# Performance work log

Hardware: AMD Instinct MI355X
Metric: run time of the kernel (lower is better)

## Reference

```python
import jax, jax.numpy as jnp
import numpy as np

INPUT_DIM, HIDDEN, OUTPUT_DIM, NUM_LAYERS = 512, 128, 96, 5
BATCH, SEQ = 64, 512


def _gru_layer(x_seq, w_ih, w_hh, b_ih, b_hh):
    """Single GRU layer, PyTorch gate conventions. x_seq: [B,T,I] -> [B,T,H]."""
    B = x_seq.shape[0]
    H = w_hh.shape[1]
    # Precompute input-to-hidden gates for all timesteps: [B,T,3H]
    gx = jnp.einsum('bti,gi->btg', x_seq, w_ih) + b_ih

    def step(h, gx_t):
        gh = h @ w_hh.T + b_hh                      # [B,3H]
        xr, xz, xn = jnp.split(gx_t, 3, axis=-1)
        hr, hz, hn = jnp.split(gh, 3, axis=-1)
        r = jax.nn.sigmoid(xr + hr)
        z = jax.nn.sigmoid(xz + hz)
        n = jnp.tanh(xn + r * hn)
        h_new = (1.0 - z) * n + z * h
        return h_new, h_new

    h0 = jnp.zeros((B, H), x_seq.dtype)
    _, hs = jax.lax.scan(step, h0, jnp.swapaxes(gx, 0, 1))  # [T,B,H]
    return jnp.swapaxes(hs, 0, 1)                           # [B,T,H]


def setup_inputs() -> dict:
    key = jax.random.key(0)
    ks = jax.random.split(key, 8)
    s = 1.0 / np.sqrt(HIDDEN)  # torch default uniform init bound
    u = lambda k, shape: jax.random.uniform(k, shape, jnp.float32, -s, s)
    return {
        'x': jax.random.normal(ks[0], (BATCH, SEQ, INPUT_DIM), jnp.float32),
        'w_ih0': u(ks[1], (3 * HIDDEN, INPUT_DIM)),
        'w_ih_rest': u(ks[2], (NUM_LAYERS - 1, 3 * HIDDEN, HIDDEN)),
        'w_hh': u(ks[3], (NUM_LAYERS, 3 * HIDDEN, HIDDEN)),
        'b_ih': u(ks[4], (NUM_LAYERS, 3 * HIDDEN)),
        'b_hh': u(ks[5], (NUM_LAYERS, 3 * HIDDEN)),
        'fc_w': u(ks[6], (OUTPUT_DIM, HIDDEN)),
        'fc_b': u(ks[7], (OUTPUT_DIM,)),
    }


def reference(x, w_ih0, w_ih_rest, w_hh, b_ih, b_hh, fc_w, fc_b):
    h = _gru_layer(x, w_ih0, w_hh[0], b_ih[0], b_hh[0])
    for l in range(1, NUM_LAYERS):
        h = _gru_layer(h, w_ih_rest[l - 1], w_hh[l], b_ih[l], b_hh[l])
    # final linear on last timestep: [B,H] -> [B,OUTPUT_DIM]
    return h[:, -1, :] @ fc_w.T + fc_b
```

## Files before the change

### kernel.cpp

```cpp
#include <hip/hip_runtime.h>
#include <hip/hip_bf16.h>

#define BATCH   64
#define SEQ     512
#define IN0     512
#define HID     128
#define G3      384
#define NLAY    5
#define CHUNK   8

typedef _Float16 f16x8 __attribute__((ext_vector_type(8)));
typedef float    f32x4 __attribute__((ext_vector_type(4)));

static __device__ __forceinline__ float sigf(float x) {
    return __builtin_amdgcn_rcpf(1.f + __expf(-x));
}
static __device__ __forceinline__ float tanh_fast(float x) {
    const float e = __expf(-2.f * fabsf(x));
    return copysignf((1.f - e) * __builtin_amdgcn_rcpf(1.f + e), x);
}

__global__ __launch_bounds__(256) void gemm_gx(const float* __restrict__ A,
                                               const float* __restrict__ W,
                                               const float* __restrict__ bias,
                                               float* __restrict__ gx)
{
    __shared__ __align__(16) _Float16 As[64][40];
    __shared__ __align__(16) _Float16 Bs[64][40];

    const int tid  = threadIdx.x;
    const int lane = tid & 63;
    const int wv   = tid >> 6;
    const int n16  = lane & 15;
    const int quad = lane >> 4;
    const int row0 = blockIdx.x * 64;
    const int col0 = blockIdx.y * 64;
    const int r    = tid >> 2;
    const int kc   = (tid & 3) * 8;

    f32x4 acc[4];
    #pragma unroll
    for (int nt = 0; nt < 4; nt++) acc[nt] = (f32x4){0.f, 0.f, 0.f, 0.f};

    for (int k0 = 0; k0 < IN0; k0 += 32) {
        {
            const float* Ap = A + (size_t)(row0 + r) * IN0 + k0 + kc;
            float4 a0 = *(const float4*)(Ap);
            float4 a1 = *(const float4*)(Ap + 4);
            f16x8 v;
            v[0] = (_Float16)a0.x; v[1] = (_Float16)a0.y; v[2] = (_Float16)a0.z; v[3] = (_Float16)a0.w;
            v[4] = (_Float16)a1.x; v[5] = (_Float16)a1.y; v[6] = (_Float16)a1.z; v[7] = (_Float16)a1.w;
            *(f16x8*)&As[r][kc] = v;
        }
        {
            const float* Wp = W + (size_t)(col0 + r) * IN0 + k0 + kc;
            float4 b0 = *(const float4*)(Wp);
            float4 b1 = *(const float4*)(Wp + 4);
            f16x8 v;
            v[0] = (_Float16)b0.x; v[1] = (_Float16)b0.y; v[2] = (_Float16)b0.z; v[3] = (_Float16)b0.w;
            v[4] = (_Float16)b1.x; v[5] = (_Float16)b1.y; v[6] = (_Float16)b1.z; v[7] = (_Float16)b1.w;
            *(f16x8*)&Bs[r][kc] = v;
        }
        __syncthreads();

        const f16x8 af = *(const f16x8*)&As[wv * 16 + n16][quad * 8];
        #pragma unroll
        for (int nt = 0; nt < 4; nt++) {
            const f16x8 bfr = *(const f16x8*)&Bs[nt * 16 + n16][quad * 8];
            acc[nt] = __builtin_amdgcn_mfma_f32_16x16x32_f16(af, bfr, acc[nt], 0, 0, 0);
        }
        __syncthreads();
    }

    #pragma unroll
    for (int nt = 0; nt < 4; nt++) {
        const int col = col0 + nt * 16 + n16;
        const float bb = bias[col];
        #pragma unroll
        for (int r4 = 0; r4 < 4; r4++) {
            const int row = row0 + wv * 16 + quad * 4 + r4;
            gx[(size_t)row * G3 + col] = acc[nt][r4] + bb;
        }
    }
}

__global__ __launch_bounds__(512, 2) void gru_pipeline(
    const float* __restrict__ gx0,
    const float* __restrict__ w_ih_rest,
    const float* __restrict__ w_hh,
    const float* __restrict__ b_ih,
    const float* __restrict__ b_hh,
    _Float16* __restrict__ hmid,
    float* __restrict__ hlast,
    int* __restrict__ flags)
{
    const int l    = blockIdx.x >> 2;
    const int g    = blockIdx.x & 3;
    const int bm0  = g * 16;
    const int tid  = threadIdx.x;
    const int lane = tid & 63;
    const int n16  = lane & 15;
    const int quad = lane >> 4;
    const int wv   = tid >> 6;
    const int j    = wv * 16 + n16;

    __shared__ __align__(16) _Float16 hA[2][16][136];
    __shared__ __align__(16) _Float16 hC[CHUNK][16][136];
    __shared__ int barcnt;

    f16x8 bf[3][4];
    {
        const float* wb = w_hh + (size_t)l * G3 * HID;
        #pragma unroll
        for (int tau = 0; tau < 3; tau++)
            #pragma unroll
            for (int kc = 0; kc < 4; kc++) {
                const float* wp = wb + (size_t)(tau * 128 + j) * HID + kc * 32 + quad * 8;
                f16x8 v;
                #pragma unroll
                for (int i = 0; i < 8; i++) v[i] = (_Float16)wp[i];
                bf[tau][kc] = v;
            }
    }
    f16x8 bi[3][4];
    if (l > 0) {
        const float* wb = w_ih_rest + (size_t)(l - 1) * G3 * HID;
        #pragma unroll
        for (int tau = 0; tau < 3; tau++)
            #pragma unroll
            for (int kc = 0; kc < 4; kc++) {
                const float* wp = wb + (size_t)(tau * 128 + j) * HID + kc * 32 + quad * 8;
                f16x8 v;
                #pragma unroll
                for (int i = 0; i < 8; i++) v[i] = (_Float16)wp[i];
                bi[tau][kc] = v;
            }
    }
    const float bcr = b_hh[l * G3 + j]       + ((l > 0) ? b_ih[l * G3 + j]       : 0.f);
    const float bcz = b_hh[l * G3 + j + 128] + ((l > 0) ? b_ih[l * G3 + j + 128] : 0.f);
    const float bcn = b_hh[l * G3 + j + 256];
    const float bxn = (l > 0) ? b_ih[l * G3 + j + 256] : 0.f;

    for (int i = tid; i < 2 * 16 * 136; i += 512) ((_Float16*)hA)[i] = (_Float16)0.f;
    float vhp[4] = {0.f, 0.f, 0.f, 0.f};
    if (tid == 0) barcnt = 0;

    const float* pR[4];
    float xr[4], xz[4], xn[4];
    if (l == 0) {
        #pragma unroll
        for (int r = 0; r < 4; r++) {
            pR[r] = gx0 + (size_t)(bm0 + quad * 4 + r) * SEQ * G3 + j;
            xr[r] = pR[r][0]; xz[r] = pR[r][128]; xn[r] = pR[r][256];
            pR[r] += G3;
        }
    }

    const _Float16* hprev = (l > 0) ? hmid + (size_t)((l - 1) * 4 + g) * SEQ * 2048 : (const _Float16*)nullptr;
    _Float16*       hpub  = (l < 4) ? hmid + (size_t)(l * 4 + g) * SEQ * 2048 : (_Float16*)nullptr;
    int*       dstflag = (l < 4) ? &flags[l * 4 + g] : (int*)nullptr;
    const int* srcflag = (l > 0) ? &flags[(l - 1) * 4 + g] : (const int*)nullptr;

    f16x8 ap[4];
    const int hoff = n16 * 128 + quad * 8;

    __syncthreads();

    volatile int* bc = &barcnt;
    int btarget = 0;

    for (int c = 0; c < SEQ / CHUNK; c++) {
        const int t0 = c * CHUNK;

        if (l > 0) {
            const int need = t0 + CHUNK;
            int v = __hip_atomic_load(srcflag, __ATOMIC_RELAXED, __HIP_MEMORY_SCOPE_AGENT);
            while (v < need) {
                __builtin_amdgcn_s_sleep(2);
                v = __hip_atomic_load(srcflag, __ATOMIC_RELAXED, __HIP_MEMORY_SCOPE_AGENT);
            }
            (void)__hip_atomic_load(srcflag, __ATOMIC_ACQUIRE, __HIP_MEMORY_SCOPE_AGENT);
            __asm__ volatile("" ::: "memory");
            const _Float16* hp = hprev + (size_t)t0 * 2048 + hoff;
            #pragma unroll
            for (int kc = 0; kc < 4; kc++) ap[kc] = *(const f16x8*)(hp + kc * 32);
        }

        #pragma unroll
        for (int i = 0; i < CHUNK; i++) {
            const int t = t0 + i;

            __asm__ volatile("" ::: "memory");
            if (lane == 0) atomicAdd(&barcnt, 1);
            btarget += 8;
            while (*bc < btarget) { __builtin_amdgcn_s_sleep(1); }
            __asm__ volatile("" ::: "memory");

            const int buf = t & 1;
            f16x8 af[4];
            #pragma unroll
            for (int kc = 0; kc < 4; kc++)
                af[kc] = *(const f16x8*)&hA[buf][n16][kc * 32 + quad * 8];

            f32x4 ai0 = {0.f,0.f,0.f,0.f}, ai1 = ai0, ai2 = ai0;
            if (l > 0) {
                #pragma unroll
                for (int kc = 0; kc < 4; kc++) {
                    ai0 = __builtin_amdgcn_mfma_f32_16x16x32_f16(ap[kc], bi[0][kc], ai0, 0, 0, 0);
                    ai1 = __builtin_amdgcn_mfma_f32_16x16x32_f16(ap[kc], bi[1][kc], ai1, 0, 0, 0);
                    ai2 = __builtin_amdgcn_mfma_f32_16x16x32_f16(ap[kc], bi[2][kc], ai2, 0, 0, 0);
                }
            }

            if (l > 0 && i < CHUNK - 1) {
                const _Float16* hp = hprev + (size_t)(t + 1) * 2048 + hoff;
                #pragma unroll
                for (int kc = 0; kc < 4; kc++) ap[kc] = *(const f16x8*)(hp + kc * 32);
            }

            float nr[4], nz[4], nn[4];
            if (l == 0) {
                #pragma unroll
                for (int r = 0; r < 4; r++) {
                    nr[r] = pR[r][0]; nz[r] = pR[r][128]; nn[r] = pR[r][256];
                }
                if (t + 1 < SEQ) {
                    #pragma unroll
                    for (int r = 0; r < 4; r++) pR[r] += G3;
                }
            }

            f32x4 ah0 = {0.f,0.f,0.f,0.f}, ah1 = ah0, ah2 = ah0;
            #pragma unroll
            for (int kc = 0; kc < 4; kc++) {
                ah0 = __builtin_amdgcn_mfma_f32_16x16x32_f16(af[kc], bf[0][kc], ah0, 0, 0, 0);
                ah1 = __builtin_amdgcn_mfma_f32_16x16x32_f16(af[kc], bf[1][kc], ah1, 0, 0, 0);
                ah2 = __builtin_amdgcn_mfma_f32_16x16x32_f16(af[kc], bf[2][kc], ah2, 0, 0, 0);
            }

            const int nbuf = buf ^ 1;
            #pragma unroll
            for (int r = 0; r < 4; r++) {
                const float sxr = (l == 0) ? xr[r] : ai0[r];
                const float sxz = (l == 0) ? xz[r] : ai1[r];
                const float sxn = ((l == 0) ? xn[r] : ai2[r]) + bxn;
                const float rg  = sigf(sxr + ah0[r] + bcr);
                const float zg  = sigf(sxz + ah1[r] + bcz);
                const float th  = tanh_fast(sxn + rg * (ah2[r] + bcn));
                const float hnew = fmaf(zg, vhp[r] - th, th);
                vhp[r] = hnew;
                hA[nbuf][quad * 4 + r][j] = (_Float16)hnew;
                if (l < 4) hC[i][quad * 4 + r][j] = (_Float16)hnew;
                if (l == 4 && t == SEQ - 1)
                    hlast[(bm0 + quad * 4 + r) * 128 + j] = hnew;
            }

            if (l == 0) {
                #pragma unroll
                for (int r = 0; r < 4; r++) { xr[r] = nr[r]; xz[r] = nz[r]; xn[r] = nn[r]; }
            }
        }

        __syncthreads();
        if (l < 4) {
            _Float16* dstc = hpub + (size_t)t0 * 2048;
            f16x8 v0, v1, v2, v3;
            {
                const int seg0 = tid;
                const int seg1 = tid + 512;
                const int seg2 = tid + 1024;
                const int seg3 = tid + 1536;
                v0 = *(const f16x8*)&hC[(seg0 >> 8)][(seg0 >> 4) & 15][(seg0 & 15) * 8];
                v1 = *(const f16x8*)&hC[(seg1 >> 8)][(seg1 >> 4) & 15][(seg1 & 15) * 8];
                v2 = *(const f16x8*)&hC[(seg2 >> 8)][(seg2 >> 4) & 15][(seg2 & 15) * 8];
                v3 = *(const f16x8*)&hC[(seg3 >> 8)][(seg3 >> 4) & 15][(seg3 & 15) * 8];
                *(f16x8*)(dstc + (seg0 >> 4) * 128 + (seg0 & 15) * 8) = v0;
                *(f16x8*)(dstc + (seg1 >> 4) * 128 + (seg1 & 15) * 8) = v1;
                *(f16x8*)(dstc + (seg2 >> 4) * 128 + (seg2 & 15) * 8) = v2;
                *(f16x8*)(dstc + (seg3 >> 4) * 128 + (seg3 & 15) * 8) = v3;
            }
        }
        __syncthreads();
        if (l < 4 && tid == 0)
            __hip_atomic_store(dstflag, t0 + CHUNK, __ATOMIC_RELEASE, __HIP_MEMORY_SCOPE_AGENT);
    }
}

__global__ __launch_bounds__(128) void fc_kernel(const float* __restrict__ hlast,
                                                 const float* __restrict__ fc_w,
                                                 const float* __restrict__ fc_b,
                                                 float* __restrict__ out)
{
    const int b = blockIdx.x;
    const int o = threadIdx.x;
    if (o < 96) {
        const float* h = hlast + (size_t)b * HID;
        const float* wrow = fc_w + o * HID;
        float acc = fc_b[o];
        #pragma unroll 4
        for (int k = 0; k < HID; k++) acc = fmaf(h[k], wrow[k], acc);
        out[b * 96 + o] = acc;
    }
}

extern "C" void kernel_launch(void* const* d_in, const int* in_sizes, int n_in,
                              void* d_out, int out_size, void* d_ws, size_t ws_size,
                              hipStream_t stream)
{
    const float* x         = (const float*)d_in[0];
    const float* w_ih0     = (const float*)d_in[1];
    const float* w_ih_rest = (const float*)d_in[2];
    const float* w_hh      = (const float*)d_in[3];
    const float* b_ih      = (const float*)d_in[4];
    const float* b_hh      = (const float*)d_in[5];
    const float* fc_w      = (const float*)d_in[6];
    const float* fc_b      = (const float*)d_in[7];
    float* out = (float*)d_out;

    int*      flags = (int*)d_ws;
    float*    gxbuf = (float*)((char*)d_ws + 256);
    _Float16* hmid  = (_Float16*)((char*)d_ws + 256 + 50331648);
    float*    hlast = (float*)((char*)d_ws + 256 + 50331648 + 33554432);

    hipMemsetAsync(d_ws, 0, 256, stream);

    const dim3 gemmGrid(512, 6);
    gemm_gx<<<gemmGrid, 256, 0, stream>>>(x, w_ih0, b_ih, gxbuf);

    gru_pipeline<<<NLAY * 4, 512, 0, stream>>>(gxbuf, w_ih_rest, w_hh, b_ih, b_hh,
                                               hmid, hlast, flags);

    fc_kernel<<<BATCH, 128, 0, stream>>>(hlast, fc_w, fc_b, out);
}
```

Before: 903.9 us.

## Merge hidden-state LDS buffers and use per-wave release flags between layers

```diff
diff --git a/kernel.cpp b/kernel.cpp
--- a/kernel.cpp
+++ b/kernel.cpp
@@ -16,7 +16,7 @@
     return __builtin_amdgcn_rcpf(1.f + __expf(-x));
 }
 static __device__ __forceinline__ float tanh_fast(float x) {
-    const float e = __expf(-2.f * fabsf(x));
+    const float e = exp2f(fabsf(x) * -2.885390082f);
     return copysignf((1.f - e) * __builtin_amdgcn_rcpf(1.f + e), x);
 }
 
@@ -104,8 +104,7 @@
     const int wv   = tid >> 6;
     const int j    = wv * 16 + n16;
 
-    __shared__ __align__(16) _Float16 hA[2][16][136];
-    __shared__ __align__(16) _Float16 hC[CHUNK][16][136];
+    __shared__ __align__(16) _Float16 hS[CHUNK][16][136];
     __shared__ int barcnt;
 
     f16x8 bf[3][4];
@@ -141,7 +140,7 @@
     const float bcn = b_hh[l * G3 + j + 256];
     const float bxn = (l > 0) ? b_ih[l * G3 + j + 256] : 0.f;
 
-    for (int i = tid; i < 2 * 16 * 136; i += 512) ((_Float16*)hA)[i] = (_Float16)0.f;
+    for (int i = tid; i < CHUNK * 16 * 136; i += 512) ((_Float16*)hS)[i] = (_Float16)0.f;
     float vhp[4] = {0.f, 0.f, 0.f, 0.f};
     if (tid == 0) barcnt = 0;
 
@@ -173,7 +172,7 @@
         const int t0 = c * CHUNK;
 
         if (l > 0) {
-            const int need = t0 + CHUNK;
+            const int need = (c + 1) * 8;
             int v = __hip_atomic_load(srcflag, __ATOMIC_RELAXED, __HIP_MEMORY_SCOPE_AGENT);
             while (v < need) {
                 __builtin_amdgcn_s_sleep(2);
@@ -196,13 +195,14 @@
             while (*bc < btarget) { __builtin_amdgcn_s_sleep(1); }
             __asm__ volatile("" ::: "memory");
 
-            const int buf = t & 1;
+            const int rb = (i + CHUNK - 1) & (CHUNK - 1);
             f16x8 af[4];
             #pragma unroll
             for (int kc = 0; kc < 4; kc++)
-                af[kc] = *(const f16x8*)&hA[buf][n16][kc * 32 + quad * 8];
-
-            f32x4 ai0 = {0.f,0.f,0.f,0.f}, ai1 = ai0, ai2 = ai0;
+                af[kc] = *(const f16x8*)&hS[rb][n16][kc * 32 + quad * 8];
+
+            f32x4 ai0 = {0.f, 0.f, 0.f, 0.f}, ai1 = ai0;
+            f32x4 ai2 = {bxn, bxn, bxn, bxn};
             if (l > 0) {
                 #pragma unroll
                 for (int kc = 0; kc < 4; kc++) {
@@ -230,7 +230,9 @@
                 }
             }
 
-            f32x4 ah0 = {0.f,0.f,0.f,0.f}, ah1 = ah0, ah2 = ah0;
+            f32x4 ah0 = {bcr, bcr, bcr, bcr};
+            f32x4 ah1 = {bcz, bcz, bcz, bcz};
+            f32x4 ah2 = {bcn, bcn, bcn, bcn};
             #pragma unroll
             for (int kc = 0; kc < 4; kc++) {
                 ah0 = __builtin_amdgcn_mfma_f32_16x16x32_f16(af[kc], bf[0][kc], ah0, 0, 0, 0);
@@ -238,19 +240,17 @@
                 ah2 = __builtin_amdgcn_mfma_f32_16x16x32_f16(af[kc], bf[2][kc], ah2, 0, 0, 0);
             }
 
-            const int nbuf = buf ^ 1;
             #pragma unroll
             for (int r = 0; r < 4; r++) {
                 const float sxr = (l == 0) ? xr[r] : ai0[r];
                 const float sxz = (l == 0) ? xz[r] : ai1[r];
-                const float sxn = ((l == 0) ? xn[r] : ai2[r]) + bxn;
-                const float rg  = sigf(sxr + ah0[r] + bcr);
-                const float zg  = sigf(sxz + ah1[r] + bcz);
-                const float th  = tanh_fast(sxn + rg * (ah2[r] + bcn));
+                const float sxn = (l == 0) ? xn[r] : ai2[r];
+                const float rg  = sigf(sxr + ah0[r]);
+                const float zg  = sigf(sxz + ah1[r]);
+                const float th  = tanh_fast(fmaf(rg, ah2[r], sxn));
                 const float hnew = fmaf(zg, vhp[r] - th, th);
                 vhp[r] = hnew;
-                hA[nbuf][quad * 4 + r][j] = (_Float16)hnew;
-                if (l < 4) hC[i][quad * 4 + r][j] = (_Float16)hnew;
+                hS[i][quad * 4 + r][j] = (_Float16)hnew;
                 if (l == 4 && t == SEQ - 1)
                     hlast[(bm0 + quad * 4 + r) * 128 + j] = hnew;
             }
@@ -261,28 +261,27 @@
             }
         }
 
-        __syncthreads();
         if (l < 4) {
+            __syncthreads();
             _Float16* dstc = hpub + (size_t)t0 * 2048;
-            f16x8 v0, v1, v2, v3;
             {
                 const int seg0 = tid;
                 const int seg1 = tid + 512;
                 const int seg2 = tid + 1024;
                 const int seg3 = tid + 1536;
-                v0 = *(const f16x8*)&hC[(seg0 >> 8)][(seg0 >> 4) & 15][(seg0 & 15) * 8];
-                v1 = *(const f16x8*)&hC[(seg1 >> 8)][(seg1 >> 4) & 15][(seg1 & 15) * 8];
-                v2 = *(const f16x8*)&hC[(seg2 >> 8)][(seg2 >> 4) & 15][(seg2 & 15) * 8];
-                v3 = *(const f16x8*)&hC[(seg3 >> 8)][(seg3 >> 4) & 15][(seg3 & 15) * 8];
+                f16x8 v0 = *(const f16x8*)&hS[(seg0 >> 8)][(seg0 >> 4) & 15][(seg0 & 15) * 8];
+                f16x8 v1 = *(const f16x8*)&hS[(seg1 >> 8)][(seg1 >> 4) & 15][(seg1 & 15) * 8];
+                f16x8 v2 = *(const f16x8*)&hS[(seg2 >> 8)][(seg2 >> 4) & 15][(seg2 & 15) * 8];
+                f16x8 v3 = *(const f16x8*)&hS[(seg3 >> 8)][(seg3 >> 4) & 15][(seg3 & 15) * 8];
                 *(f16x8*)(dstc + (seg0 >> 4) * 128 + (seg0 & 15) * 8) = v0;
                 *(f16x8*)(dstc + (seg1 >> 4) * 128 + (seg1 & 15) * 8) = v1;
                 *(f16x8*)(dstc + (seg2 >> 4) * 128 + (seg2 & 15) * 8) = v2;
                 *(f16x8*)(dstc + (seg3 >> 4) * 128 + (seg3 & 15) * 8) = v3;
             }
-        }
-        __syncthreads();
-        if (l < 4 && tid == 0)
-            __hip_atomic_store(dstflag, t0 + CHUNK, __ATOMIC_RELEASE, __HIP_MEMORY_SCOPE_AGENT);
+            __asm__ volatile("s_waitcnt vmcnt(0)" ::: "memory");
+            if (lane == 0)
+                __hip_atomic_fetch_add(dstflag, 1, __ATOMIC_RELEASE, __HIP_MEMORY_SCOPE_AGENT);
+        }
     }
 }
 
```

New measurement: 1.342 ms. 48.4% more time.
